# Performance work log

Hardware: AMD Instinct MI355X
Metric: run time of the kernel (lower is better)

## Reference

```python
import jax, jax.numpy as jnp
import numpy as np

B, T, E = 4, 2048, 512
H, D = 8, 64            # num_heads, head_size = E // H
HID = H * E             # FFN hidden = num_heads * n_embed (per source)
EPS = 1e-5


def layer_norm(x, g, b):
    mu = jnp.mean(x, axis=-1, keepdims=True)
    var = jnp.var(x, axis=-1, keepdims=True)
    return (x - mu) * jax.lax.rsqrt(var + EPS) * g + b


def setup_inputs() -> dict:
    key = jax.random.key(0)
    ks = jax.random.split(key, 12)
    s_e = 1.0 / np.sqrt(E)
    s_hd = 1.0 / np.sqrt(H * D)
    s_hid = 1.0 / np.sqrt(HID)
    return {
        "x": jax.random.normal(ks[0], (B, T, E), jnp.float32),
        "Wq": jax.random.normal(ks[1], (H, E, D), jnp.float32) * s_e,
        "Wk": jax.random.normal(ks[2], (H, E, D), jnp.float32) * s_e,
        "Wv": jax.random.normal(ks[3], (H, E, D), jnp.float32) * s_e,
        "Wo": jax.random.normal(ks[4], (H * D, E), jnp.float32) * s_hd,
        "bo": jnp.zeros((E,), jnp.float32),
        "W1": jax.random.normal(ks[5], (E, HID), jnp.float32) * s_e,
        "b1": jnp.zeros((HID,), jnp.float32),
        "W2": jax.random.normal(ks[6], (HID, E), jnp.float32) * s_hid,
        "b2": jnp.zeros((E,), jnp.float32),
        "g1": jnp.ones((E,), jnp.float32),
        "be1": jnp.zeros((E,), jnp.float32),
        "g2": jnp.ones((E,), jnp.float32),
        "be2": jnp.zeros((E,), jnp.float32),
    }


def reference(x, Wq, Wk, Wv, Wo, bo, W1, b1, W2, b2, g1, be1, g2, be2):
    # pre-LN decoder block (layer_norm_first=True path)
    xn = layer_norm(x, g1, be1)

    # multi-head causal attention; NOTE: scale is T**-0.5 per the source code
    q = jnp.einsum('bte,hed->bhtd', xn, Wq)
    k = jnp.einsum('bte,hed->bhtd', xn, Wk)
    v = jnp.einsum('bte,hed->bhtd', xn, Wv)
    scores = jnp.einsum('bhtd,bhsd->bhts', q, k) * (T ** -0.5)
    causal = jnp.tril(jnp.ones((T, T), bool))
    scores = jnp.where(causal, scores, -jnp.inf)
    attn = jax.nn.softmax(scores, axis=-1)
    o = jnp.einsum('bhts,bhsd->bhtd', attn, v)           # [B,H,T,D]
    o = o.transpose(0, 2, 1, 3).reshape(B, T, H * D)      # concat heads
    mha = o @ Wo + bo

    x = xn + mha
    xn2 = layer_norm(x, g2, be2)
    ffn = jax.nn.relu(xn2 @ W1 + b1) @ W2 + b2
    return xn2 + ffn
```

## Files before the change

kernel.cpp:

```cpp
#include <hip/hip_runtime.h>
#include <hip/hip_bf16.h>
#include <math.h>

#define Bsz 4
#define Tt 2048
#define Ee 512
#define Hh 8
#define Dd 64
#define HIDs 4096
#define Mrows (Bsz * Tt)

typedef __attribute__((ext_vector_type(8))) short short8;
typedef __attribute__((ext_vector_type(4))) float f32x4;

#define AS1 __attribute__((address_space(1)))
#define AS3 __attribute__((address_space(3)))

__device__ __forceinline__ unsigned short f2bfu(float f) {
    unsigned u = __float_as_uint(f);
    return (unsigned short)((u + 0x7fffu + ((u >> 16) & 1u)) >> 16);
}
__device__ __forceinline__ unsigned short truncbf(float f) {
    return (unsigned short)(__float_as_uint(f) >> 16);
}

__global__ __launch_bounds__(256) void ln_kernel(const float* __restrict__ x,
        const float* __restrict__ g, const float* __restrict__ b,
        const float* __restrict__ addb,
        float* __restrict__ out_f, __hip_bfloat16* __restrict__ out_bf) {
    int row = blockIdx.x;
    int tid = threadIdx.x;
    const float* xr = x + (size_t)row * Ee;
    float v0 = xr[tid];
    float v1 = xr[tid + 256];
    float s = v0 + v1;
    float sq = v0 * v0 + v1 * v1;
#pragma unroll
    for (int off = 32; off > 0; off >>= 1) {
        s  += __shfl_xor(s, off, 64);
        sq += __shfl_xor(sq, off, 64);
    }
    __shared__ float ls[4], lq[4];
    int wid = tid >> 6, lane = tid & 63;
    if (lane == 0) { ls[wid] = s; lq[wid] = sq; }
    __syncthreads();
    s  = ls[0] + ls[1] + ls[2] + ls[3];
    sq = lq[0] + lq[1] + lq[2] + lq[3];
    float mean = s * (1.0f / Ee);
    float var  = sq * (1.0f / Ee) - mean * mean;
    float rstd = rsqrtf(var + 1e-5f);
    float o0 = (v0 - mean) * rstd * g[tid]       + b[tid];
    float o1 = (v1 - mean) * rstd * g[tid + 256] + b[tid + 256];
    float* orow = out_f + (size_t)row * Ee;
    orow[tid]       = o0 + addb[tid];
    orow[tid + 256] = o1 + addb[tid + 256];
    __hip_bfloat16* brow = out_bf + (size_t)row * Ee;
    brow[tid]       = __float2bfloat16(o0);
    brow[tid + 256] = __float2bfloat16(o1);
}

__device__ __forceinline__ void tr_tile(const float* __restrict__ in,
        __hip_bfloat16* __restrict__ outp, int R, int C, int c0, int r0) {
    __shared__ float tile[64][65];
    int tc = threadIdx.x & 63, tg = threadIdx.x >> 6;
#pragma unroll
    for (int i = 0; i < 16; ++i) {
        int r = tg * 16 + i;
        tile[r][tc] = in[(size_t)(r0 + r) * C + c0 + tc];
    }
    __syncthreads();
#pragma unroll
    for (int i = 0; i < 16; ++i) {
        int cc = tg * 16 + i;
        outp[(size_t)(c0 + cc) * R + r0 + tc] = __float2bfloat16(tile[tc][cc]);
    }
}
__global__ __launch_bounds__(256) void repack_all(const float* __restrict__ Wq,
        const float* __restrict__ Wk, const float* __restrict__ Wv,
        const float* __restrict__ Wo, const float* __restrict__ W1,
        const float* __restrict__ W2, __hip_bfloat16* __restrict__ bqT,
        __hip_bfloat16* __restrict__ woT, __hip_bfloat16* __restrict__ w1T,
        __hip_bfloat16* __restrict__ w2T) {
    int blk = blockIdx.x;
    if (blk < 192) {
        int p = blk >> 6, h = (blk >> 3) & 7, et = blk & 7;
        const float* W = (p == 0) ? Wq : ((p == 1) ? Wk : Wv);
        float sc = (p == 0) ? 0.022097086912079608f * 1.4426950408889634f : 1.0f;
        __shared__ float tile[64][65];
        int td = threadIdx.x & 63, tg = threadIdx.x >> 6;
#pragma unroll
        for (int i = 0; i < 16; ++i) {
            int e = tg * 16 + i;
            tile[e][td] = W[((size_t)h * Ee + et * 64 + e) * Dd + td] * sc;
        }
        __syncthreads();
#pragma unroll
        for (int i = 0; i < 16; ++i) {
            int d = tg * 16 + i;
            bqT[((size_t)(p * 512 + h * 64 + d)) * Ee + et * 64 + td] =
                __float2bfloat16(tile[td][d]);
        }
    } else if (blk < 256) {
        int t = blk - 192;
        tr_tile(Wo, woT, 512, 512, (t & 7) * 64, (t >> 3) * 64);
    } else if (blk < 768) {
        int t = blk - 256;
        tr_tile(W1, w1T, 512, HIDs, (t & 63) * 64, (t >> 6) * 64);
    } else {
        int t = blk - 768;
        tr_tile(W2, w2T, HIDs, 512, (t & 7) * 64, (t >> 3) * 64);
    }
}

__global__ __launch_bounds__(256) void mfma_gemm(
        const __hip_bfloat16* __restrict__ A, int lda,
        const __hip_bfloat16* __restrict__ B, int ldb,
        __hip_bfloat16* __restrict__ Cb, int ldc, int K, int nx) {
    __shared__ __hip_bfloat16 As[2 * 128 * 32];
    __shared__ __hip_bfloat16 Bs[2 * 128 * 32];
    int tid = threadIdx.x;
    int lane = tid & 63, wave = tid >> 6;
    int wm = wave >> 1, wn = wave & 1;
    int L = blockIdx.x;
    int slots = (int)gridDim.x >> 3;
    int v = (L & 7) * slots + (L >> 3);
    int bx = v % nx, by = v / nx;
    int row0 = by * 128, col0 = bx * 128;
    f32x4 acc[4][4];
#pragma unroll
    for (int i = 0; i < 4; ++i)
#pragma unroll
        for (int j = 0; j < 4; ++j) acc[i][j] = (f32x4){0.f, 0.f, 0.f, 0.f};

    int fr = lane & 15;
    int kq = (lane >> 4) << 3;

    for (int k0 = 0; k0 < K; k0 += 64) {
        __syncthreads();
#pragma unroll
        for (int j = 0; j < 4; ++j) {
            int c  = j * 256 + tid;
            int cb = j * 256 + wave * 64;
            int p  = c >> 9, cp = c & 511;
            int r  = cp >> 2, kg = (cp & 3) << 3;
            int ko = k0 + p * 32 + kg;
            __builtin_amdgcn_global_load_lds(
                (const AS1 void*)(A + (size_t)(row0 + r) * lda + ko),
                (AS3 void*)(As + cb * 8), 16, 0, 0);
            __builtin_amdgcn_global_load_lds(
                (const AS1 void*)(B + (size_t)(col0 + r) * ldb + ko),
                (AS3 void*)(Bs + cb * 8), 16, 0, 0);
        }
        __syncthreads();
#pragma unroll
        for (int ks = 0; ks < 2; ++ks) {
            short8 afr[4], bfr[4];
#pragma unroll
            for (int i = 0; i < 4; ++i) {
                afr[i] = *(const short8*)(As + ks * 4096 + (wm * 64 + i * 16 + fr) * 32 + kq);
                bfr[i] = *(const short8*)(Bs + ks * 4096 + (wn * 64 + i * 16 + fr) * 32 + kq);
            }
#pragma unroll
            for (int i = 0; i < 4; ++i)
#pragma unroll
                for (int j = 0; j < 4; ++j)
                    acc[i][j] = __builtin_amdgcn_mfma_f32_16x16x32_bf16(afr[i], bfr[j], acc[i][j], 0, 0, 0);
        }
    }
    int rq = (lane >> 4) << 2;
#pragma unroll
    for (int i = 0; i < 4; ++i)
#pragma unroll
        for (int j = 0; j < 4; ++j)
#pragma unroll
            for (int gidx = 0; gidx < 4; ++gidx) {
                int r = row0 + wm * 64 + i * 16 + rq + gidx;
                int c = col0 + wn * 64 + j * 16 + fr;
                Cb[(size_t)r * ldc + c] = __float2bfloat16(acc[i][j][gidx]);
            }
}

__global__ __launch_bounds__(256) void mfma_gemm_n64(
        const __hip_bfloat16* __restrict__ A, int lda,
        const __hip_bfloat16* __restrict__ B, int ldb,
        float* __restrict__ Cf, int ldc, int K, int nx) {
    __shared__ __hip_bfloat16 As[2 * 128 * 32];
    __shared__ __hip_bfloat16 Bs[2 * 64 * 32];
    int tid = threadIdx.x;
    int lane = tid & 63, wave = tid >> 6;
    int L = blockIdx.x;
    int slots = (int)gridDim.x >> 3;
    int v = (L & 7) * slots + (L >> 3);
    int bx = v % nx, by = v / nx;
    int row0 = by * 128, col0 = bx * 64;
    f32x4 acc[2][4];
#pragma unroll
    for (int i = 0; i < 2; ++i)
#pragma unroll
        for (int j = 0; j < 4; ++j) acc[i][j] = (f32x4){0.f, 0.f, 0.f, 0.f};

    int fr = lane & 15;
    int kq = (lane >> 4) << 3;

    for (int k0 = 0; k0 < K; k0 += 64) {
        __syncthreads();
#pragma unroll
        for (int j = 0; j < 4; ++j) {
            int c  = j * 256 + tid;
            int cb = j * 256 + wave * 64;
            int p  = c >> 9, cp = c & 511;
            int r  = cp >> 2, kg = (cp & 3) << 3;
            __builtin_amdgcn_global_load_lds(
                (const AS1 void*)(A + (size_t)(row0 + r) * lda + k0 + p * 32 + kg),
                (AS3 void*)(As + cb * 8), 16, 0, 0);
        }
#pragma unroll
        for (int j = 0; j < 2; ++j) {
            int c  = j * 256 + tid;
            int cb = j * 256 + wave * 64;
            int p  = c >> 8, cp = c & 255;
            int r  = cp >> 2, kg = (cp & 3) << 3;
            __builtin_amdgcn_global_load_lds(
                (const AS1 void*)(B + (size_t)(col0 + r) * ldb + k0 + p * 32 + kg),
                (AS3 void*)(Bs + cb * 8), 16, 0, 0);
        }
        __syncthreads();
#pragma unroll
        for (int ks = 0; ks < 2; ++ks) {
            short8 afr[2], bfr[4];
#pragma unroll
            for (int i = 0; i < 2; ++i)
                afr[i] = *(const short8*)(As + ks * 4096 + (wave * 32 + i * 16 + fr) * 32 + kq);
#pragma unroll
            for (int j = 0; j < 4; ++j)
                bfr[j] = *(const short8*)(Bs + ks * 2048 + (j * 16 + fr) * 32 + kq);
#pragma unroll
            for (int i = 0; i < 2; ++i)
#pragma unroll
                for (int j = 0; j < 4; ++j)
                    acc[i][j] = __builtin_amdgcn_mfma_f32_16x16x32_bf16(afr[i], bfr[j], acc[i][j], 0, 0, 0);
        }
    }
    int rq = (lane >> 4) << 2;
#pragma unroll
    for (int i = 0; i < 2; ++i)
#pragma unroll
        for (int j = 0; j < 4; ++j)
#pragma unroll
            for (int gidx = 0; gidx < 4; ++gidx) {
                int r = row0 + wave * 32 + i * 16 + rq + gidx;
                int c = col0 + j * 16 + fr;
                Cf[(size_t)r * ldc + c] += acc[i][j][gidx];
            }
}

__global__ __launch_bounds__(256) void mfma_gemm256(
        const __hip_bfloat16* __restrict__ A, int lda,
        const __hip_bfloat16* __restrict__ B, int ldb,
        __hip_bfloat16* __restrict__ Cb, int ldc, int K,
        const float* __restrict__ bias) {
    __shared__ __hip_bfloat16 As[2 * 256 * 32];
    __shared__ __hip_bfloat16 Bs[2 * 128 * 32];
    int tid = threadIdx.x;
    int lane = tid & 63, wave = tid >> 6;
    int L = blockIdx.x;
    int k8 = L & 7, sub = L >> 3;
    int sr = k8 >> 1, sc = k8 & 1;
    int by = sr * 8 + (sub >> 4);
    int bx = sc * 16 + (sub & 15);
    int row0 = by * 256, col0 = bx * 128;
    f32x4 acc[4][8];
#pragma unroll
    for (int i = 0; i < 4; ++i)
#pragma unroll
        for (int j = 0; j < 8; ++j) acc[i][j] = (f32x4){0.f, 0.f, 0.f, 0.f};

    int fr = lane & 15;
    int kq = (lane >> 4) << 3;
    int nsteps = K >> 5;

#define STAGE256(st, buf)                                                     \
    do {                                                                      \
        int ko_ = (st) << 5;                                                  \
        _Pragma("unroll")                                                     \
        for (int j = 0; j < 4; ++j) {                                         \
            int c = j * 256 + tid;                                            \
            int cb = j * 256 + wave * 64;                                     \
            int r = c >> 2, kg = (c & 3) << 3;                                \
            __builtin_amdgcn_global_load_lds(                                 \
                (const AS1 void*)(A + (size_t)(row0 + r) * lda + ko_ + kg),   \
                (AS3 void*)(As + (buf) * 8192 + cb * 8), 16, 0, 0);           \
        }                                                                     \
        _Pragma("unroll")                                                     \
        for (int j = 0; j < 2; ++j) {                                         \
            int c = j * 256 + tid;                                            \
            int cb = j * 256 + wave * 64;                                     \
            int r = c >> 2, kg = (c & 3) << 3;                                \
            __builtin_amdgcn_global_load_lds(                                 \
                (const AS1 void*)(B + (size_t)(col0 + r) * ldb + ko_ + kg),   \
                (AS3 void*)(Bs + (buf) * 4096 + cb * 8), 16, 0, 0);           \
        }                                                                     \
    } while (0)

    STAGE256(0, 0);
    __syncthreads();
    for (int st = 0; st < nsteps; ++st) {
        int buf = st & 1;
        if (st + 1 < nsteps) STAGE256(st + 1, buf ^ 1);
        short8 afr[4], bfr[8];
#pragma unroll
        for (int i = 0; i < 4; ++i)
            afr[i] = *(const short8*)(As + buf * 8192 + (wave * 64 + i * 16 + fr) * 32 + kq);
#pragma unroll
        for (int j = 0; j < 8; ++j)
            bfr[j] = *(const short8*)(Bs + buf * 4096 + (j * 16 + fr) * 32 + kq);
#pragma unroll
        for (int i = 0; i < 4; ++i)
#pragma unroll
            for (int j = 0; j < 8; ++j)
                acc[i][j] = __builtin_amdgcn_mfma_f32_16x16x32_bf16(afr[i], bfr[j], acc[i][j], 0, 0, 0);
        __syncthreads();
    }
#undef STAGE256

    int rq = (lane >> 4) << 2;
    float bv[8];
#pragma unroll
    for (int j = 0; j < 8; ++j) bv[j] = bias[col0 + j * 16 + fr];
#pragma unroll
    for (int i = 0; i < 4; ++i)
#pragma unroll
        for (int j = 0; j < 8; ++j)
#pragma unroll
            for (int gidx = 0; gidx < 4; ++gidx) {
                int r = row0 + wave * 64 + i * 16 + rq + gidx;
                int c = col0 + j * 16 + fr;
                float t = acc[i][j][gidx] + bv[j];
                Cb[(size_t)r * ldc + c] = __float2bfloat16(t > 0.f ? t : 0.f);
            }
}

__global__ __launch_bounds__(512) void attn_mfma(const __hip_bfloat16* __restrict__ qkvb,
        __hip_bfloat16* __restrict__ ob) {
    __shared__ __hip_bfloat16 KsS[64 * 72];
    __shared__ __hip_bfloat16 VtS[64 * 72];
    __shared__ __hip_bfloat16 PsS[8 * 16 * 72];
    __hip_bfloat16* Qs = PsS;

    const unsigned short* q16 = (const unsigned short*)qkvb;
    int tid  = threadIdx.x;
    int lane = tid & 63, wave = tid >> 6;
    int g = lane >> 4, c = lane & 15;
    int blk = blockIdx.x;
    int qb  = 15 - (blk >> 5);
    int bh  = blk & 31;
    int b = bh >> 3, h = bh & 7;
    int base = qb * 128;
    size_t tokbase = (size_t)b * Tt;
    int qoff = h * 64, koff = 512 + h * 64, voff = 1024 + h * 64;

    {
        int q = tid >> 2, dg = (tid & 3) * 16;
        const unsigned short* src = q16 + (tokbase + base + q) * 1536 + qoff + dg;
        uint4 a  = *(const uint4*)src;
        uint4 b4 = *(const uint4*)(src + 8);
        *(uint4*)(Qs + q * 72 + dg)     = a;
        *(uint4*)(Qs + q * 72 + dg + 8) = b4;
    }
    __syncthreads();
    short8 aq[2];
    aq[0] = *(const short8*)(Qs + (wave * 16 + c) * 72 + g * 8);
    aq[1] = *(const short8*)(Qs + (wave * 16 + c) * 72 + 32 + g * 8);

    short8 ones;
#pragma unroll
    for (int i = 0; i < 8; ++i) ones[i] = (short)0x3F80;

    f32x4 acc[4];
#pragma unroll
    for (int dt = 0; dt < 4; ++dt) acc[dt] = (f32x4){0.f, 0.f, 0.f, 0.f};
    f32x4 accL = (f32x4){0.f, 0.f, 0.f, 0.f};
    __hip_bfloat16* Psw = PsS + wave * (16 * 72);
    unsigned short* Psw16 = (unsigned short*)Psw;

    int s_k = tid >> 3, dg_k = (tid & 7) * 8;
    int sp = (tid & 31) * 2, dg4 = (tid >> 5) * 4;
    uint4 kreg; uint2 va, vb;
    {
        kreg = *(const uint4*)(q16 + (tokbase + s_k) * 1536 + koff + dg_k);
        const unsigned short* r0p = q16 + (tokbase + sp) * 1536 + voff + dg4;
        va = *(const uint2*)r0p;
        vb = *(const uint2*)(r0p + 1536);
    }

    int tmax = 2 * qb + 1;
    for (int tile = 0; tile <= tmax; ++tile) {
        __syncthreads();
        *(uint4*)(KsS + s_k * 72 + dg_k) = kreg;
        {
            unsigned a0[2] = {va.x, va.y};
            unsigned b0[2] = {vb.x, vb.y};
#pragma unroll
            for (int i = 0; i < 2; ++i) {
                unsigned p0 = (a0[i] & 0xffffu) | (b0[i] << 16);
                unsigned p1 = (a0[i] >> 16) | (b0[i] & 0xffff0000u);
                *(unsigned*)(VtS + (dg4 + 2 * i) * 72 + sp)     = p0;
                *(unsigned*)(VtS + (dg4 + 2 * i + 1) * 72 + sp) = p1;
            }
        }
        __syncthreads();
        if (tile < tmax) {
            int s1 = (tile + 1) * 64;
            kreg = *(const uint4*)(q16 + (tokbase + s1 + s_k) * 1536 + koff + dg_k);
            const unsigned short* r0p = q16 + (tokbase + s1 + sp) * 1536 + voff + dg4;
            va = *(const uint2*)r0p;
            vb = *(const uint2*)(r0p + 1536);
        }
        if (tile == tmax && wave < 4) continue;
        f32x4 Sc[4];
#pragma unroll
        for (int st = 0; st < 4; ++st) Sc[st] = (f32x4){0.f, 0.f, 0.f, 0.f};
#pragma unroll
        for (int ks = 0; ks < 2; ++ks)
#pragma unroll
            for (int st = 0; st < 4; ++st) {
                short8 bk = *(const short8*)(KsS + (st * 16 + c) * 72 + ks * 32 + g * 8);
                Sc[st] = __builtin_amdgcn_mfma_f32_16x16x32_bf16(aq[ks], bk, Sc[st], 0, 0, 0);
            }
        if (tile >= 2 * qb) {
            int s0 = tile * 64;
            int qg = base + wave * 16 + g * 4;
#pragma unroll
            for (int st = 0; st < 4; ++st) {
                int sg = s0 + st * 16 + c;
#pragma unroll
                for (int r = 0; r < 4; ++r)
                    if (sg > qg + r) Sc[st][r] = -1e30f;
            }
        }
#pragma unroll
        for (int st = 0; st < 4; ++st)
#pragma unroll
            for (int r = 0; r < 4; ++r)
                Psw16[(g * 4 + r) * 72 + st * 16 + c] =
                    truncbf(__builtin_amdgcn_exp2f(Sc[st][r]));
#pragma unroll
        for (int ks = 0; ks < 2; ++ks) {
            short8 ap = *(const short8*)(Psw + c * 72 + ks * 32 + g * 8);
            accL = __builtin_amdgcn_mfma_f32_16x16x32_bf16(ap, ones, accL, 0, 0, 0);
#pragma unroll
            for (int dt = 0; dt < 4; ++dt) {
                short8 bv = *(const short8*)(VtS + (dt * 16 + c) * 72 + ks * 32 + g * 8);
                acc[dt] = __builtin_amdgcn_mfma_f32_16x16x32_bf16(ap, bv, acc[dt], 0, 0, 0);
            }
        }
    }
    float rl[4];
#pragma unroll
    for (int r = 0; r < 4; ++r) rl[r] = 1.0f / accL[r];
#pragma unroll
    for (int dt = 0; dt < 4; ++dt)
#pragma unroll
        for (int r = 0; r < 4; ++r) {
            int row = base + wave * 16 + g * 4 + r;
            float o = acc[dt][r] * rl[r];
            ob[(tokbase + row) * 512 + h * 64 + dt * 16 + c] = __float2bfloat16(o);
        }
}

extern "C" void kernel_launch(void* const* d_in, const int* in_sizes, int n_in,
                              void* d_out, int out_size, void* d_ws, size_t ws_size,
                              hipStream_t stream) {
    const float* x   = (const float*)d_in[0];
    const float* Wq  = (const float*)d_in[1];
    const float* Wk  = (const float*)d_in[2];
    const float* Wv  = (const float*)d_in[3];
    const float* Wo  = (const float*)d_in[4];
    const float* bo  = (const float*)d_in[5];
    const float* W1  = (const float*)d_in[6];
    const float* b1  = (const float*)d_in[7];
    const float* W2  = (const float*)d_in[8];
    const float* b2  = (const float*)d_in[9];
    const float* g1  = (const float*)d_in[10];
    const float* be1 = (const float*)d_in[11];
    const float* g2  = (const float*)d_in[12];
    const float* be2 = (const float*)d_in[13];
    float* out = (float*)d_out;

    char* ws = (char*)d_ws;
    __hip_bfloat16* bqT    = (__hip_bfloat16*)(ws);
    __hip_bfloat16* woT    = (__hip_bfloat16*)(ws + 1572864);
    __hip_bfloat16* w1T    = (__hip_bfloat16*)(ws + 2097152);
    __hip_bfloat16* w2T    = (__hip_bfloat16*)(ws + 6291456);
    float*          xn     = (float*)(ws + 10485760);
    __hip_bfloat16* xn_bf  = (__hip_bfloat16*)(ws + 27262976);
    __hip_bfloat16* qkv_bf = (__hip_bfloat16*)(ws + 35651584);
    __hip_bfloat16* o_bf   = (__hip_bfloat16*)(ws + 60817408);
    __hip_bfloat16* h_bf   = (__hip_bfloat16*)(ws + 35651584);

    ln_kernel<<<Mrows, 256, 0, stream>>>(x, g1, be1, bo, xn, xn_bf);
    repack_all<<<1280, 256, 0, stream>>>(Wq, Wk, Wv, Wo, W1, W2, bqT, woT, w1T, w2T);
    mfma_gemm<<<768, 256, 0, stream>>>(
        xn_bf, 512, bqT, 512, qkv_bf, 1536, 512, 12);
    attn_mfma<<<Bsz * Hh * (Tt / 128), 512, 0, stream>>>(qkv_bf, o_bf);
    mfma_gemm_n64<<<512, 256, 0, stream>>>(
        o_bf, 512, woT, 512, xn, 512, 512, 8);
    ln_kernel<<<Mrows, 256, 0, stream>>>(xn, g2, be2, b2, out, xn_bf);
    mfma_gemm256<<<1024, 256, 0, stream>>>(
        xn_bf, 512, w1T, 512, h_bf, HIDs, 512, b1);
    mfma_gemm_n64<<<512, 256, 0, stream>>>(
        h_bf, HIDs, w2T, HIDs, out, 512, HIDs, 8);
}
```

Before: 342.3 us.

## Merge startup kernels, stage GEMM epilogues through LDS, single-buffer FFN1 GEMM

Fuses the first layernorm and weight repack into one launch to save a kernel launch and let both run concurrently. The QKV and FFN1 GEMM epilogues now write bf16 tiles into shared memory and then store them to global as 16-byte vectors, replacing scattered 2-byte stores. The 256-row FFN1 GEMM drops its double-buffered pipeline for a single buffer with two barriers per step. That shrinks LDS use but loses the overlap of loads with MFMA work.

```diff
diff --git a/kernel.cpp b/kernel.cpp
--- a/kernel.cpp
+++ b/kernel.cpp
@@ -24,11 +24,11 @@
     return (unsigned short)(__float_as_uint(f) >> 16);
 }
 
-__global__ __launch_bounds__(256) void ln_kernel(const float* __restrict__ x,
+__device__ __forceinline__ void ln_body(const float* __restrict__ x,
         const float* __restrict__ g, const float* __restrict__ b,
         const float* __restrict__ addb,
-        float* __restrict__ out_f, __hip_bfloat16* __restrict__ out_bf) {
-    int row = blockIdx.x;
+        float* __restrict__ out_f, __hip_bfloat16* __restrict__ out_bf,
+        int row) {
     int tid = threadIdx.x;
     const float* xr = x + (size_t)row * Ee;
     float v0 = xr[tid];
@@ -59,6 +59,13 @@
     brow[tid + 256] = __float2bfloat16(o1);
 }
 
+__global__ __launch_bounds__(256) void ln_kernel(const float* __restrict__ x,
+        const float* __restrict__ g, const float* __restrict__ b,
+        const float* __restrict__ addb,
+        float* __restrict__ out_f, __hip_bfloat16* __restrict__ out_bf) {
+    ln_body(x, g, b, addb, out_f, out_bf, blockIdx.x);
+}
+
 __device__ __forceinline__ void tr_tile(const float* __restrict__ in,
         __hip_bfloat16* __restrict__ outp, int R, int C, int c0, int r0) {
     __shared__ float tile[64][65];
@@ -75,13 +82,20 @@
         outp[(size_t)(c0 + cc) * R + r0 + tc] = __float2bfloat16(tile[tc][cc]);
     }
 }
-__global__ __launch_bounds__(256) void repack_all(const float* __restrict__ Wq,
-        const float* __restrict__ Wk, const float* __restrict__ Wv,
-        const float* __restrict__ Wo, const float* __restrict__ W1,
-        const float* __restrict__ W2, __hip_bfloat16* __restrict__ bqT,
-        __hip_bfloat16* __restrict__ woT, __hip_bfloat16* __restrict__ w1T,
-        __hip_bfloat16* __restrict__ w2T) {
-    int blk = blockIdx.x;
+__global__ __launch_bounds__(256) void startup_kernel(
+        const float* __restrict__ x, const float* __restrict__ g1,
+        const float* __restrict__ be1, const float* __restrict__ bo,
+        float* __restrict__ xn, __hip_bfloat16* __restrict__ xn_bf,
+        const float* __restrict__ Wq, const float* __restrict__ Wk,
+        const float* __restrict__ Wv, const float* __restrict__ Wo,
+        const float* __restrict__ W1, const float* __restrict__ W2,
+        __hip_bfloat16* __restrict__ bqT, __hip_bfloat16* __restrict__ woT,
+        __hip_bfloat16* __restrict__ w1T, __hip_bfloat16* __restrict__ w2T) {
+    if (blockIdx.x < Mrows) {
+        ln_body(x, g1, be1, bo, xn, xn_bf, blockIdx.x);
+        return;
+    }
+    int blk = blockIdx.x - Mrows;
     if (blk < 192) {
         int p = blk >> 6, h = (blk >> 3) & 7, et = blk & 7;
         const float* W = (p == 0) ? Wq : ((p == 1) ? Wk : Wv);
@@ -116,8 +130,9 @@
         const __hip_bfloat16* __restrict__ A, int lda,
         const __hip_bfloat16* __restrict__ B, int ldb,
         __hip_bfloat16* __restrict__ Cb, int ldc, int K, int nx) {
-    __shared__ __hip_bfloat16 As[2 * 128 * 32];
-    __shared__ __hip_bfloat16 Bs[2 * 128 * 32];
+    __shared__ __hip_bfloat16 S[16384];
+    __hip_bfloat16* As = S;
+    __hip_bfloat16* Bs = S + 8192;
     int tid = threadIdx.x;
     int lane = tid & 63, wave = tid >> 6;
     int wm = wave >> 1, wn = wave & 1;
@@ -167,17 +182,24 @@
                     acc[i][j] = __builtin_amdgcn_mfma_f32_16x16x32_bf16(afr[i], bfr[j], acc[i][j], 0, 0, 0);
         }
     }
+    __syncthreads();
+    unsigned short* Ew = (unsigned short*)S + wave * 1152;
+    const __hip_bfloat16* Er = (const __hip_bfloat16*)Ew;
     int rq = (lane >> 4) << 2;
-#pragma unroll
-    for (int i = 0; i < 4; ++i)
+    int rr = lane >> 2, cb2 = (lane & 3) * 16;
+#pragma unroll
+    for (int i = 0; i < 4; ++i) {
 #pragma unroll
         for (int j = 0; j < 4; ++j)
 #pragma unroll
-            for (int gidx = 0; gidx < 4; ++gidx) {
-                int r = row0 + wm * 64 + i * 16 + rq + gidx;
-                int c = col0 + wn * 64 + j * 16 + fr;
-                Cb[(size_t)r * ldc + c] = __float2bfloat16(acc[i][j][gidx]);
-            }
+            for (int gi = 0; gi < 4; ++gi)
+                Ew[(rq + gi) * 72 + j * 16 + fr] = f2bfu(acc[i][j][gi]);
+        uint4 v0 = *(const uint4*)(Er + rr * 72 + cb2);
+        uint4 v1 = *(const uint4*)(Er + rr * 72 + cb2 + 8);
+        size_t rg = (size_t)(row0 + wm * 64 + i * 16 + rr) * ldc + col0 + wn * 64 + cb2;
+        *(uint4*)(Cb + rg)     = v0;
+        *(uint4*)(Cb + rg + 8) = v1;
+    }
 }
 
 __global__ __launch_bounds__(256) void mfma_gemm_n64(
@@ -259,8 +281,9 @@
         const __hip_bfloat16* __restrict__ B, int ldb,
         __hip_bfloat16* __restrict__ Cb, int ldc, int K,
         const float* __restrict__ bias) {
-    __shared__ __hip_bfloat16 As[2 * 256 * 32];
-    __shared__ __hip_bfloat16 Bs[2 * 128 * 32];
+    __shared__ __hip_bfloat16 S[12288];
+    __hip_bfloat16* As = S;
+    __hip_bfloat16* Bs = S + 8192;
     int tid = threadIdx.x;
     int lane = tid & 63, wave = tid >> 6;
     int L = blockIdx.x;
@@ -277,67 +300,63 @@
 
     int fr = lane & 15;
     int kq = (lane >> 4) << 3;
-    int nsteps = K >> 5;
-
-#define STAGE256(st, buf)                                                     \
-    do {                                                                      \
-        int ko_ = (st) << 5;                                                  \
-        _Pragma("unroll")                                                     \
-        for (int j = 0; j < 4; ++j) {                                         \
-            int c = j * 256 + tid;                                            \
-            int cb = j * 256 + wave * 64;                                     \
-            int r = c >> 2, kg = (c & 3) << 3;                                \
-            __builtin_amdgcn_global_load_lds(                                 \
-                (const AS1 void*)(A + (size_t)(row0 + r) * lda + ko_ + kg),   \
-                (AS3 void*)(As + (buf) * 8192 + cb * 8), 16, 0, 0);           \
-        }                                                                     \
-        _Pragma("unroll")                                                     \
-        for (int j = 0; j < 2; ++j) {                                         \
-            int c = j * 256 + tid;                                            \
-            int cb = j * 256 + wave * 64;                                     \
-            int r = c >> 2, kg = (c & 3) << 3;                                \
-            __builtin_amdgcn_global_load_lds(                                 \
-                (const AS1 void*)(B + (size_t)(col0 + r) * ldb + ko_ + kg),   \
-                (AS3 void*)(Bs + (buf) * 4096 + cb * 8), 16, 0, 0);           \
-        }                                                                     \
-    } while (0)
-
-    STAGE256(0, 0);
-    __syncthreads();
-    for (int st = 0; st < nsteps; ++st) {
-        int buf = st & 1;
-        if (st + 1 < nsteps) STAGE256(st + 1, buf ^ 1);
+
+    for (int k0 = 0; k0 < K; k0 += 32) {
+        __syncthreads();
+#pragma unroll
+        for (int j = 0; j < 4; ++j) {
+            int c  = j * 256 + tid;
+            int cb = j * 256 + wave * 64;
+            int r = c >> 2, kg = (c & 3) << 3;
+            __builtin_amdgcn_global_load_lds(
+                (const AS1 void*)(A + (size_t)(row0 + r) * lda + k0 + kg),
+                (AS3 void*)(As + cb * 8), 16, 0, 0);
+        }
+#pragma unroll
+        for (int j = 0; j < 2; ++j) {
+            int c  = j * 256 + tid;
+            int cb = j * 256 + wave * 64;
+            int r = c >> 2, kg = (c & 3) << 3;
+            __builtin_amdgcn_global_load_lds(
+                (const AS1 void*)(B + (size_t)(col0 + r) * ldb + k0 + kg),
+                (AS3 void*)(Bs + cb * 8), 16, 0, 0);
+        }
+        __syncthreads();
         short8 afr[4], bfr[8];
 #pragma unroll
         for (int i = 0; i < 4; ++i)
-            afr[i] = *(const short8*)(As + buf * 8192 + (wave * 64 + i * 16 + fr) * 32 + kq);
+            afr[i] = *(const short8*)(As + (wave * 64 + i * 16 + fr) * 32 + kq);
 #pragma unroll
         for (int j = 0; j < 8; ++j)
-            bfr[j] = *(const short8*)(Bs + buf * 4096 + (j * 16 + fr) * 32 + kq);
+            bfr[j] = *(const short8*)(Bs + (j * 16 + fr) * 32 + kq);
 #pragma unroll
         for (int i = 0; i < 4; ++i)
 #pragma unroll
             for (int j = 0; j < 8; ++j)
                 acc[i][j] = __builtin_amdgcn_mfma_f32_16x16x32_bf16(afr[i], bfr[j], acc[i][j], 0, 0, 0);
-        __syncthreads();
-    }
-#undef STAGE256
-
+    }
+    __syncthreads();
+    float bv[8];
+#pragma unroll
+    for (int j = 0; j < 8; ++j) bv[j] = bias[col0 + j * 16 + fr];
+    unsigned short* Ew = (unsigned short*)S + wave * 2176;
+    const __hip_bfloat16* Er = (const __hip_bfloat16*)Ew;
     int rq = (lane >> 4) << 2;
-    float bv[8];
-#pragma unroll
-    for (int j = 0; j < 8; ++j) bv[j] = bias[col0 + j * 16 + fr];
-#pragma unroll
-    for (int i = 0; i < 4; ++i)
+    int rr = lane >> 2, cb2 = (lane & 3) * 32;
+#pragma unroll
+    for (int i = 0; i < 4; ++i) {
 #pragma unroll
         for (int j = 0; j < 8; ++j)
 #pragma unroll
-            for (int gidx = 0; gidx < 4; ++gidx) {
-                int r = row0 + wave * 64 + i * 16 + rq + gidx;
-                int c = col0 + j * 16 + fr;
-                float t = acc[i][j][gidx] + bv[j];
-                Cb[(size_t)r * ldc + c] = __float2bfloat16(t > 0.f ? t : 0.f);
-            }
+            for (int gi = 0; gi < 4; ++gi) {
+                float t = acc[i][j][gi] + bv[j];
+                Ew[(rq + gi) * 136 + j * 16 + fr] = f2bfu(t > 0.f ? t : 0.f);
+            }
+        size_t rg = (size_t)(row0 + wave * 64 + i * 16 + rr) * ldc + col0 + cb2;
+#pragma unroll
+        for (int u = 0; u < 4; ++u)
+            *(uint4*)(Cb + rg + u * 8) = *(const uint4*)(Er + rr * 136 + cb2 + u * 8);
+    }
 }
 
 __global__ __launch_bounds__(512) void attn_mfma(const __hip_bfloat16* __restrict__ qkvb,
@@ -498,8 +517,8 @@
     __hip_bfloat16* o_bf   = (__hip_bfloat16*)(ws + 60817408);
     __hip_bfloat16* h_bf   = (__hip_bfloat16*)(ws + 35651584);
 
-    ln_kernel<<<Mrows, 256, 0, stream>>>(x, g1, be1, bo, xn, xn_bf);
-    repack_all<<<1280, 256, 0, stream>>>(Wq, Wk, Wv, Wo, W1, W2, bqT, woT, w1T, w2T);
+    startup_kernel<<<Mrows + 1280, 256, 0, stream>>>(
+        x, g1, be1, bo, xn, xn_bf, Wq, Wk, Wv, Wo, W1, W2, bqT, woT, w1T, w2T);
     mfma_gemm<<<768, 256, 0, stream>>>(
         xn_bf, 512, bqT, 512, qkv_bf, 1536, 512, 12);
     attn_mfma<<<Bsz * Hh * (Tt / 128), 512, 0, stream>>>(qkv_bf, o_bf);
```

After: 361.3 us. +5.5%, slower.
